# Optimization experiments

Hardware: AMD Instinct MI355X
Metric: run time of the kernel (lower is better)

Reference implementation:

```python
import jax, jax.numpy as jnp
import numpy as np

S, C = 4096, 12            # words per sentence, chars per word
V, NC = 50000, 26          # word vocab, char vocab
E, EC = 1024, 256          # word / char embedding dims
H, HC = 1024, 256          # word / char LSTM hidden dims
T = 64                     # tagset size


def _lstm_step(W_ih, W_hh, b_ih, b_hh, carry, x):
    # PyTorch LSTM gate order: i, f, g, o
    h, c = carry
    gates = x @ W_ih.T + h @ W_hh.T + b_ih + b_hh
    i, f, g, o = jnp.split(gates, 4, axis=-1)
    c = jax.nn.sigmoid(f) * c + jax.nn.sigmoid(i) * jnp.tanh(g)
    h = jax.nn.sigmoid(o) * jnp.tanh(c)
    return (h, c), h


def setup_inputs() -> dict:
    key = jax.random.key(0)
    ks = jax.random.split(key, 16)
    s = 0.02
    return {
        "char_idx": jax.random.randint(ks[0], (S, C), 0, NC),
        "word_idx": jax.random.randint(ks[1], (S,), 0, V),
        "W_emb_word": jax.random.normal(ks[2], (V, E), jnp.float32) * s,
        "W_emb_char": jax.random.normal(ks[3], (NC, EC), jnp.float32) * s,
        "W_ih_c": jax.random.normal(ks[4], (4 * HC, EC), jnp.float32) * s,
        "W_hh_c": jax.random.normal(ks[5], (4 * HC, HC), jnp.float32) * s,
        "b_ih_c": jnp.zeros((4 * HC,), jnp.float32),
        "b_hh_c": jnp.zeros((4 * HC,), jnp.float32),
        "W_ih": jax.random.normal(ks[6], (4 * H, E + HC), jnp.float32) * s,
        "W_hh": jax.random.normal(ks[7], (4 * H, H), jnp.float32) * s,
        "b_ih": jnp.zeros((4 * H,), jnp.float32),
        "b_hh": jnp.zeros((4 * H,), jnp.float32),
        "W_tag": jax.random.normal(ks[8], (T, H), jnp.float32) * s,
        "b_tag": jnp.zeros((T,), jnp.float32),
    }


def reference(char_idx, word_idx, W_emb_word, W_emb_char,
              W_ih_c, W_hh_c, b_ih_c, b_hh_c,
              W_ih, W_hh, b_ih, b_hh, W_tag, b_tag):
    # --- char-level LSTM, batched over all S words at once ---
    char_x = W_emb_char[char_idx]                     # [S, C, EC]
    carry0 = (jnp.zeros((S, HC), char_x.dtype), jnp.zeros((S, HC), char_x.dtype))
    step_c = lambda carry, x: _lstm_step(W_ih_c, W_hh_c, b_ih_c, b_hh_c, carry, x)
    (h_char, _), _ = jax.lax.scan(step_c, carry0, jnp.swapaxes(char_x, 0, 1))  # h_char: [S, HC]

    # --- word-level LSTM over the sentence (batch 1) ---
    word_emb = W_emb_word[word_idx]                   # [S, E]
    x = jnp.concatenate([word_emb, h_char], axis=-1)  # [S, E+HC]
    carry0w = (jnp.zeros((H,), x.dtype), jnp.zeros((H,), x.dtype))
    step_w = lambda carry, xt: _lstm_step(W_ih, W_hh, b_ih, b_hh, carry, xt)
    _, hs = jax.lax.scan(step_w, carry0w, x)          # hs: [S, H]

    tag_space = hs @ W_tag.T + b_tag                  # [S, T]
    return jax.nn.log_softmax(tag_space, axis=1)
```

## Files before the change

kernel.cpp:

```cpp
#include <hip/hip_runtime.h>
#include <hip/hip_bf16.h>

#define SLEN 4096
#define CLEN 12
#define ECD  256
#define HCD  256
#define ED   1024
#define HD   1024
#define TD   64
#define NSLOT 32
#define POLL_LIMIT 2048

typedef unsigned  uv4 __attribute__((ext_vector_type(4)));
typedef __attribute__((ext_vector_type(8))) short bf16x8;
typedef __attribute__((ext_vector_type(4))) float f32x4;

#if defined(__has_builtin)
#if __has_builtin(__builtin_amdgcn_sdot4)
#define HAVE_SDOT4 1
#endif
#if __has_builtin(__builtin_amdgcn_perm)
#define HAVE_PERM 1
#endif
#endif

#ifdef HAVE_PERM
#define PERM2(hi, lo) __builtin_amdgcn_perm((unsigned)(hi), (unsigned)(lo), 0x05040100u)
#else
#define PERM2(hi, lo) ((((unsigned)(lo)) & 0xFFFFu) | (((unsigned)(hi)) << 16))
#endif

#define GLOAD_LDS16(g, l)                                                    \
    __builtin_amdgcn_global_load_lds(                                        \
        (const __attribute__((address_space(1))) void*)(g),                  \
        (__attribute__((address_space(3))) void*)(l), 16, 0, 0)

__device__ __forceinline__ float sigmoidf_(float x) { return 1.f / (1.f + __expf(-x)); }
__device__ __forceinline__ float tanh_fast(float x) {
    float ax = fabsf(x);
    float e = __expf(2.f * ax);
    float t = 1.f - 2.f / (e + 1.f);
    return copysignf(t, x);
}
__device__ __forceinline__ unsigned short bf16r(float f) {
    unsigned u = __float_as_uint(f);
    return (unsigned short)((u + 0x7FFFu + ((u >> 16) & 1u)) >> 16);
}

__global__ __launch_bounds__(256) void prep_all(
    const float* __restrict__ Wih,  unsigned short* __restrict__ Wihb,
    const float* __restrict__ Wec,  const float* __restrict__ Wihc,
    const float* __restrict__ bihc, const float* __restrict__ bhhc,
    float* __restrict__ table,
    const float* __restrict__ Whhc, unsigned short* __restrict__ Wt,
    const float* __restrict__ Wtag, unsigned short* __restrict__ Wtagb,
    unsigned* __restrict__ hdata, int* __restrict__ xcd_ctr,
    const int* __restrict__ word_idx, const float* __restrict__ Wemb,
    unsigned short* __restrict__ Xw)
{
    const int b = blockIdx.x, tid = threadIdx.x;
    if (b < 2560) {
        int i = b * 256 + tid;
        const float4* s = reinterpret_cast<const float4*>(Wih + (size_t)i * 8);
        float4 a = s[0], b2 = s[1];
        unsigned short o[8] = { bf16r(a.x), bf16r(a.y), bf16r(a.z), bf16r(a.w),
                                bf16r(b2.x), bf16r(b2.y), bf16r(b2.z), bf16r(b2.w) };
        *reinterpret_cast<uint4*>(Wihb + (size_t)i * 8) = *reinterpret_cast<uint4*>(o);
    } else if (b < 2664) {
        int id = (b - 2560) * 256 + tid;
        if (id < 26 * 1024) {
            int c = id >> 10, rp = id & 1023;
            int u = rp >> 2, g = rp & 3, row = g * 256 + u;
            const float4* a = reinterpret_cast<const float4*>(Wec + (size_t)c * 256);
            const float4* bb = reinterpret_cast<const float4*>(Wihc + (size_t)row * 256);
            float acc = 0.f;
            #pragma unroll 16
            for (int k = 0; k < 64; ++k) {
                float4 av = a[k], bv = bb[k];
                acc += av.x * bv.x + av.y * bv.y + av.z * bv.z + av.w * bv.w;
            }
            table[id] = acc + bihc[row] + bhhc[row];
        }
    } else if (b < 2792) {
        int id = (b - 2664) * 256 + tid;
        int C = id >> 5, kg = id & 31;
        int h = C >> 9, rem = C & 511, g = rem >> 7, ul = rem & 127;
        int row = g * 256 + h * 128 + ul;
        const float4* sv = reinterpret_cast<const float4*>(
            Whhc + (size_t)row * 256 + kg * 8);
        float4 a = sv[0], b2 = sv[1];
        unsigned short o[8] = { bf16r(a.x), bf16r(a.y), bf16r(a.z), bf16r(a.w),
                                bf16r(b2.x), bf16r(b2.y), bf16r(b2.z), bf16r(b2.w) };
        *reinterpret_cast<uint4*>(Wt + (size_t)(kg * 1024 + C) * 8) =
            *reinterpret_cast<uint4*>(o);
    } else if (b < 2824) {
        int i = (b - 2792) * 256 + tid;
        const float4* s = reinterpret_cast<const float4*>(Wtag + (size_t)i * 8);
        float4 a = s[0], b2 = s[1];
        unsigned short o[8] = { bf16r(a.x), bf16r(a.y), bf16r(a.z), bf16r(a.w),
                                bf16r(b2.x), bf16r(b2.y), bf16r(b2.z), bf16r(b2.w) };
        *reinterpret_cast<uint4*>(Wtagb + (size_t)i * 8) = *reinterpret_cast<uint4*>(o);
    } else if (b < 2856) {
        hdata[(b - 2824) * 256 + tid] = 0xFFFF0000u;
    } else if (b < 4904) {
        int id = (b - 2856) * 256 + tid;
        int row = id >> 7, c8 = id & 127;
        int k = c8 * 8;
        const float4* sv = reinterpret_cast<const float4*>(
            Wemb + (size_t)word_idx[row] * 1024 + k);
        float4 a = sv[0], b2 = sv[1];
        unsigned short o[8] = { bf16r(a.x), bf16r(a.y), bf16r(a.z), bf16r(a.w),
                                bf16r(b2.x), bf16r(b2.y), bf16r(b2.z), bf16r(b2.w) };
        *reinterpret_cast<uint4*>(Xw + (size_t)row * 1280 + k) =
            *reinterpret_cast<uint4*>(o);
    } else {
        if (tid < 8) xcd_ctr[tid] = 0;
    }
}

__global__ __launch_bounds__(256) void char_fused(
    const int* __restrict__ char_idx,
    const unsigned short* __restrict__ Wt,
    const float* __restrict__ table,
    unsigned short* __restrict__ Xw)
{
    __shared__ unsigned short hA[2][8192];
    __shared__ int cidx_s[32 * CLEN];

    const int tid  = threadIdx.x;
    const int lane = tid & 63;
    const int wv   = tid >> 6;
    const int fr   = lane & 15;
    const int fkq  = lane >> 4;
    const int w0   = blockIdx.x * 32;

    for (int e = tid; e < 32 * CLEN; e += 256)
        cidx_s[e] = char_idx[(w0 + (e / CLEN)) * CLEN + (e % CLEN)];
    {
        uint4 z; z.x = z.y = z.z = z.w = 0u;
        for (int e = tid; e < 1024; e += 256)
            *reinterpret_cast<uint4*>(&hA[0][e * 8]) = z;
    }
    __syncthreads();

    float cst[32];
    #pragma unroll
    for (int i = 0; i < 32; ++i) cst[i] = 0.f;

    for (int t = 0; t < CLEN; ++t) {
        const int cur = t & 1, nxt = cur ^ 1;
        #pragma unroll
        for (int h = 0; h < 2; ++h) {
            f32x4 acc[2][8];
            #pragma unroll
            for (int m = 0; m < 2; ++m)
                #pragma unroll
                for (int i = 0; i < 8; ++i) acc[m][i] = f32x4{0.f, 0.f, 0.f, 0.f};

            #pragma unroll
            for (int k0i = 0; k0i < 8; ++k0i) {
                const int kg = k0i * 4 + fkq;
                bf16x8 af[2];
                #pragma unroll
                for (int m = 0; m < 2; ++m) {
                    const int row = m * 16 + fr;
                    af[m] = *reinterpret_cast<const bf16x8*>(
                        &hA[cur][row * 256 + ((kg ^ ((row & 7) << 2)) << 3)]);
                }
                #pragma unroll
                for (int i = 0; i < 8; ++i) {
                    const int T = wv + (i << 2);
                    const int col = h * 512 + T * 16 + fr;
                    const bf16x8 bf = *reinterpret_cast<const bf16x8*>(
                        Wt + (size_t)(kg * 1024 + col) * 8);
                    acc[0][i] = __builtin_amdgcn_mfma_f32_16x16x32_bf16(
                        af[0], bf, acc[0][i], 0, 0, 0);
                    acc[1][i] = __builtin_amdgcn_mfma_f32_16x16x32_bf16(
                        af[1], bf, acc[1][i], 0, 0, 0);
                }
            }

            #pragma unroll
            for (int m = 0; m < 2; ++m) {
                #pragma unroll
                for (int r = 0; r < 4; ++r) {
                    const int wl = m * 16 + (lane >> 4) * 4 + r;
                    const int ci = cidx_s[wl * CLEN + t];
                    #pragma unroll
                    for (int ab = 0; ab < 2; ++ab) {
                        const int u = h * 128 + (wv + 4 * ab) * 16 + fr;
                        const float4 tv = *reinterpret_cast<const float4*>(
                            table + (size_t)ci * 1024 + u * 4);
                        const int cix = ((h * 2 + m) * 2 + ab) * 4 + r;
                        const float gi_ = acc[m][0 + ab][r] + tv.x;
                        const float gf_ = acc[m][2 + ab][r] + tv.y;
                        const float gg_ = acc[m][4 + ab][r] + tv.z;
                        const float go_ = acc[m][6 + ab][r] + tv.w;
                        const float i_ = sigmoidf_(gi_), f_ = sigmoidf_(gf_);
                        const float g_ = tanh_fast(gg_), o_ = sigmoidf_(go_);
                        const float cn = f_ * cst[cix] + i_ * g_;
                        cst[cix] = cn;
                        const unsigned short hb = bf16r(o_ * tanh_fast(cn));
                        const int chn = u >> 3;
                        hA[nxt][wl * 256 + ((chn ^ ((wl & 7) << 2)) << 3) + (u & 7)] = hb;
                    }
                }
            }
        }
        __syncthreads();
    }

    for (int e = tid; e < 1024; e += 256) {
        const int w = e >> 5, ch = e & 31;
        uint4 v = *reinterpret_cast<uint4*>(
            &hA[0][w * 256 + ((ch ^ ((w & 7) << 2)) << 3)]);
        *reinterpret_cast<uint4*>(
            Xw + (size_t)(w0 + w) * 1280 + 1024 + ch * 8) = v;
    }
}

__global__ __launch_bounds__(256) void gemm_bf16_bt(
    const unsigned short* __restrict__ A, const unsigned short* __restrict__ B,
    const float* __restrict__ bias0, const float* __restrict__ bias1,
    float* __restrict__ C, int M, int N, int K)
{
    __shared__ unsigned short As[128 * 64];
    __shared__ unsigned short Bs[128 * 64];
    const int tid  = threadIdx.x;
    const int lane = tid & 63;
    const int wv   = tid >> 6;
    const int wm = wv >> 1, wn = wv & 1;
    const int fr = lane & 15, fk = lane >> 4;
    const int n0 = blockIdx.x * 128;
    const int m0 = blockIdx.y * 128;

    int srcA[4], srcB[4];
    int ldsb[4];
    #pragma unroll
    for (int c = 0; c < 4; ++c) {
        int ch = c * 256 + wv * 64 + lane;
        int row = ch >> 3, chunk = ch & 7;
        int swc = chunk ^ (row & 7);
        srcA[c] = (m0 + row) * K + swc * 8;
        srcB[c] = (n0 + row) * K + swc * 8;
        ldsb[c] = (c * 256 + wv * 64) * 8;
    }

    f32x4 acc[4][4];
    #pragma unroll
    for (int i = 0; i < 4; ++i)
        #pragma unroll
        for (int j = 0; j < 4; ++j) acc[i][j] = f32x4{0.f, 0.f, 0.f, 0.f};

    for (int k0 = 0; k0 < K; k0 += 64) {
        if (k0 > 0) __syncthreads();
        #pragma unroll
        for (int c = 0; c < 4; ++c) {
            GLOAD_LDS16(A + srcA[c] + k0, As + ldsb[c]);
            GLOAD_LDS16(B + srcB[c] + k0, Bs + ldsb[c]);
        }
        asm volatile("s_waitcnt vmcnt(0)" ::: "memory");
        __syncthreads();
        #pragma unroll
        for (int ks = 0; ks < 2; ++ks) {
            bf16x8 af[4], bfr[4];
            #pragma unroll
            for (int i = 0; i < 4; ++i) {
                int ra = wm * 64 + i * 16 + fr;
                af[i] = *reinterpret_cast<const bf16x8*>(
                    &As[ra * 64 + (((ks * 4 + fk) ^ (ra & 7)) << 3)]);
                int rb = wn * 64 + i * 16 + fr;
                bfr[i] = *reinterpret_cast<const bf16x8*>(
                    &Bs[rb * 64 + (((ks * 4 + fk) ^ (rb & 7)) << 3)]);
            }
            #pragma unroll
            for (int i = 0; i < 4; ++i)
                #pragma unroll
                for (int j = 0; j < 4; ++j)
                    acc[i][j] = __builtin_amdgcn_mfma_f32_16x16x32_bf16(
                        af[i], bfr[j], acc[i][j], 0, 0, 0);
        }
    }

    const int colb = n0 + wn * 64 + fr;
    float bsum[4];
    #pragma unroll
    for (int j = 0; j < 4; ++j) bsum[j] = bias0[colb + j * 16] + bias1[colb + j * 16];
    #pragma unroll
    for (int i = 0; i < 4; ++i) {
        int row0 = m0 + wm * 64 + i * 16 + fk * 4;
        #pragma unroll
        for (int j = 0; j < 4; ++j) {
            int col = colb + j * 16;
            #pragma unroll
            for (int r = 0; r < 4; ++r)
                C[(size_t)(row0 + r) * N + col] = acc[i][j][r] + bsum[j];
        }
    }
}

__global__ __launch_bounds__(256, 1) void word_rec(
    const float* __restrict__ precomp, const float* __restrict__ W_hh,
    unsigned* __restrict__ hs_b, unsigned* hdata, int* xcd_ctr)
{
    const int tid  = threadIdx.x;
    const int v    = tid >> 6;
    const int lane = tid & 63;
    const int q    = lane >> 5;
    const int m    = lane & 31;
    const int j    = lane & 7;

    __shared__ int s_vals[2];
    if (tid == 0) {
        unsigned xcc;
        asm volatile("s_getreg_b32 %0, hwreg(HW_REG_XCC_ID)" : "=s"(xcc));
        xcc &= 7u;
        s_vals[0] = (int)xcc;
        s_vals[1] = atomicAdd(&xcd_ctr[xcc], 1);
    }
    __syncthreads();
    const int xcc  = s_vals[0];
    const int slot = s_vals[1];
    if (slot >= NSLOT) return;

    const int base_u = slot * 32 + v * 8;
    unsigned* hdata_x = hdata + xcc * 1024;

    int   wq[16][8];
    float scl[16];
    #pragma unroll
    for (int r = 0; r < 16; ++r) {
        const int grow = (2 * q + (r >> 3)) * 1024 + base_u + (r & 7);
        const float4* rp = reinterpret_cast<const float4*>(
            W_hh + (size_t)grow * 1024 + 32 * m);
        float wv_[32];
        float mx = 0.f;
        #pragma unroll
        for (int d = 0; d < 8; ++d) {
            float4 f = rp[d];
            wv_[4*d+0] = f.x; wv_[4*d+1] = f.y; wv_[4*d+2] = f.z; wv_[4*d+3] = f.w;
            mx = fmaxf(mx, fmaxf(fmaxf(fabsf(f.x), fabsf(f.y)),
                                 fmaxf(fabsf(f.z), fabsf(f.w))));
        }
        mx = fmaxf(mx, __shfl_xor(mx, 1));
        mx = fmaxf(mx, __shfl_xor(mx, 2));
        mx = fmaxf(mx, __shfl_xor(mx, 4));
        mx = fmaxf(mx, __shfl_xor(mx, 8));
        mx = fmaxf(mx, __shfl_xor(mx, 16));
        const float inv = (mx > 0.f) ? (127.f / mx) : 0.f;
        scl[r] = mx * (1.f / (127.f * 127.f));
        #pragma unroll
        for (int d = 0; d < 8; ++d) {
            int b0 = (int)rintf(wv_[4*d+0] * inv) & 255;
            int b1 = (int)rintf(wv_[4*d+1] * inv) & 255;
            int b2 = (int)rintf(wv_[4*d+2] * inv) & 255;
            int b3 = (int)rintf(wv_[4*d+3] * inv) & 255;
            wq[r][d] = b0 | (b1 << 8) | (b2 << 16) | (b3 << 24);
        }
    }

#ifdef HAVE_SDOT4
    #define DOT4(a, b, c) __builtin_amdgcn_sdot4((a), (b), (c), false)
#else
    #define DOT4(a, b, c) ({ int _d; \
        asm("v_dot4_i32_i8 %0, %1, %2, %3" : "=v"(_d) : "v"(a), "v"(b), "v"(c)); _d; })
#endif

    float c_reg = 0.f;

    for (int t = 0; t < SLEN; ++t) {
        const int pp = (t + 1) & 1;
        const int pc = t & 1;

        float pre0 = 0.f, pre1 = 0.f, pre2 = 0.f, pre3 = 0.f;
        if (lane < 8) {
            const float* pr = precomp + (size_t)t * 4096 + base_u + j;
            pre0 = pr[0]; pre1 = pr[1024]; pre2 = pr[2048]; pre3 = pr[3072];
        }

        int hq[8];
        if (t > 0) {
            const unsigned tw = ((unsigned)(t - 1)) << 16;
            const unsigned* dp = hdata_x + pp * 512 + 16 * m;
            uv4 w0_, w1_, w2_, w3_;
            int it = 0; bool dead = false;
            for (;;) {
                asm volatile(
                    "global_load_dwordx4 %0, %4, off sc0\n\t"
                    "global_load_dwordx4 %1, %4, off offset:16 sc0\n\t"
                    "global_load_dwordx4 %2, %4, off offset:32 sc0\n\t"
                    "global_load_dwordx4 %3, %4, off offset:48 sc0\n\t"
                    "s_waitcnt vmcnt(0)"
                    : "=&v"(w0_), "=&v"(w1_), "=&v"(w2_), "=&v"(w3_)
                    : "v"(dp) : "memory");
                unsigned bad =
                    (w0_.x ^ tw) | (w0_.y ^ tw) | (w0_.z ^ tw) | (w0_.w ^ tw) |
                    (w1_.x ^ tw) | (w1_.y ^ tw) | (w1_.z ^ tw) | (w1_.w ^ tw) |
                    (w2_.x ^ tw) | (w2_.y ^ tw) | (w2_.z ^ tw) | (w2_.w ^ tw) |
                    (w3_.x ^ tw) | (w3_.y ^ tw) | (w3_.z ^ tw) | (w3_.w ^ tw);
                if (__all((bad & 0xFFFF0000u) == 0u)) break;
                if (++it > POLL_LIMIT) { dead = true; break; }
            }
            if (dead) return;
            hq[0] = (int)PERM2(w0_.y, w0_.x);
            hq[1] = (int)PERM2(w0_.w, w0_.z);
            hq[2] = (int)PERM2(w1_.y, w1_.x);
            hq[3] = (int)PERM2(w1_.w, w1_.z);
            hq[4] = (int)PERM2(w2_.y, w2_.x);
            hq[5] = (int)PERM2(w2_.w, w2_.z);
            hq[6] = (int)PERM2(w3_.y, w3_.x);
            hq[7] = (int)PERM2(w3_.w, w3_.z);
        } else {
            #pragma unroll
            for (int i = 0; i < 8; ++i) hq[i] = 0;
        }

        float self = 0.f;
        #pragma unroll
        for (int r = 0; r < 16; ++r) {
            int a0 = 0, a1 = 0;
            #pragma unroll
            for (int d = 0; d < 4; ++d) {
                a0 = DOT4(wq[r][d],     hq[d],     a0);
                a1 = DOT4(wq[r][4 + d], hq[4 + d], a1);
            }
            int s = a0 + a1;
            s += __shfl_xor(s, 1);  s += __shfl_xor(s, 2);
            s += __shfl_xor(s, 4);  s += __shfl_xor(s, 8);
            s += __shfl_xor(s, 16);
            self = ((lane & 31) == r) ? (float)s * scl[r] : self;
        }

        const float gi = __shfl(self, j);
        const float gf = __shfl(self, 8 + j);
        const float gg = __shfl(self, 32 + j);
        const float go = __shfl(self, 40 + j);

        float h = 0.f;
        if (lane < 8) {
            const float i_ = sigmoidf_(gi + pre0);
            const float f_ = sigmoidf_(gf + pre1);
            const float g_ = tanh_fast(gg + pre2);
            const float o_ = sigmoidf_(go + pre3);
            c_reg = f_ * c_reg + i_ * g_;
            h = o_ * tanh_fast(c_reg);
        }

        const float hn = __shfl_down(h, 1);
        int qv = (int)rintf(fminf(fmaxf(h * 127.f, -127.f), 127.f));
        const int qn = __shfl(qv, lane | 1);
        if (lane < 8 && (lane & 1) == 0) {
            unsigned pb = (unsigned)bf16r(h) | ((unsigned)bf16r(hn) << 16);
            hs_b[(size_t)t * 512 + (base_u >> 1) + (lane >> 1)] = pb;
            unsigned pk = ((unsigned)t << 16) | ((unsigned)(qn & 255) << 8)
                        | (unsigned)(qv & 255);
            unsigned* dpw = hdata_x + pc * 512 + slot * 16 + v * 4 + (lane >> 1);
            asm volatile("global_store_dword %0, %1, off sc0"
                         :: "v"(dpw), "v"(pk) : "memory");
        }
    }
    #undef DOT4
}

__global__ __launch_bounds__(256) void tag_mfma(
    const unsigned short* __restrict__ A,
    const unsigned short* __restrict__ B,
    const float* __restrict__ btag, float* __restrict__ out)
{
    __shared__ unsigned short As[128 * 64];
    __shared__ unsigned short Bs[64 * 64];
    __shared__ float ts[128 * 65];

    const int tid  = threadIdx.x;
    const int lane = tid & 63;
    const int wm = (tid >> 6) >> 1, wn = (tid >> 6) & 1;
    const int fr = lane & 15, fk = lane >> 4;
    const int m0 = blockIdx.x * 128;

    uint4 ar[4], br[2];
    int rowa[4], kca[4], rowb[2], kcb[2];
    #pragma unroll
    for (int c = 0; c < 4; ++c) {
        int ch = c * 256 + tid;
        rowa[c] = ch >> 3; kca[c] = ch & 7;
    }
    #pragma unroll
    for (int c = 0; c < 2; ++c) {
        int ch = c * 256 + tid;
        rowb[c] = ch >> 3; kcb[c] = ch & 7;
    }

    auto load_tiles = [&](int k0) {
        #pragma unroll
        for (int c = 0; c < 4; ++c)
            ar[c] = *reinterpret_cast<const uint4*>(
                A + (size_t)(m0 + rowa[c]) * 1024 + k0 + kca[c] * 8);
        #pragma unroll
        for (int c = 0; c < 2; ++c)
            br[c] = *reinterpret_cast<const uint4*>(
                B + (size_t)rowb[c] * 1024 + k0 + kcb[c] * 8);
    };

    f32x4 acc[4][2];
    #pragma unroll
    for (int i = 0; i < 4; ++i)
        #pragma unroll
        for (int j = 0; j < 2; ++j) acc[i][j] = f32x4{0.f, 0.f, 0.f, 0.f};

    load_tiles(0);
    for (int k0 = 0; k0 < 1024; k0 += 64) {
        __syncthreads();
        #pragma unroll
        for (int c = 0; c < 4; ++c) {
            int sw = kca[c] ^ (rowa[c] & 7);
            *reinterpret_cast<uint4*>(&As[rowa[c] * 64 + sw * 8]) = ar[c];
        }
        #pragma unroll
        for (int c = 0; c < 2; ++c) {
            int sw = kcb[c] ^ (rowb[c] & 7);
            *reinterpret_cast<uint4*>(&Bs[rowb[c] * 64 + sw * 8]) = br[c];
        }
        __syncthreads();
        if (k0 + 64 < 1024) load_tiles(k0 + 64);
        #pragma unroll
        for (int ks = 0; ks < 2; ++ks) {
            bf16x8 af[4], bfr[2];
            #pragma unroll
            for (int i = 0; i < 4; ++i) {
                int ra = wm * 64 + i * 16 + fr;
                af[i] = *reinterpret_cast<const bf16x8*>(
                    &As[ra * 64 + (((ks * 4 + fk) ^ (ra & 7)) << 3)]);
            }
            #pragma unroll
            for (int j = 0; j < 2; ++j) {
                int rb = wn * 32 + j * 16 + fr;
                bfr[j] = *reinterpret_cast<const bf16x8*>(
                    &Bs[rb * 64 + (((ks * 4 + fk) ^ (rb & 7)) << 3)]);
            }
            #pragma unroll
            for (int i = 0; i < 4; ++i)
                #pragma unroll
                for (int j = 0; j < 2; ++j)
                    acc[i][j] = __builtin_amdgcn_mfma_f32_16x16x32_bf16(
                        af[i], bfr[j], acc[i][j], 0, 0, 0);
        }
    }

    #pragma unroll
    for (int i = 0; i < 4; ++i) {
        int row0 = wm * 64 + i * 16 + fk * 4;
        #pragma unroll
        for (int j = 0; j < 2; ++j) {
            int col = wn * 32 + j * 16 + fr;
            float bt = btag[col];
            #pragma unroll
            for (int r = 0; r < 4; ++r)
                ts[(row0 + r) * 65 + col] = acc[i][j][r] + bt;
        }
    }
    __syncthreads();

    if (tid < 128) {
        const float* rowp = ts + tid * 65;
        float mx = rowp[0];
        #pragma unroll 16
        for (int c = 1; c < 64; ++c) mx = fmaxf(mx, rowp[c]);
        float ssum = 0.f;
        #pragma unroll 16
        for (int c = 0; c < 64; ++c) ssum += __expf(rowp[c] - mx);
        const float lse = mx + logf(ssum);
        float* op = out + (size_t)(m0 + tid) * 64;
        #pragma unroll 16
        for (int c = 0; c < 64; ++c) op[c] = rowp[c] - lse;
    }
}

extern "C" void kernel_launch(void* const* d_in, const int* in_sizes, int n_in,
                              void* d_out, int out_size, void* d_ws, size_t ws_size,
                              hipStream_t stream)
{
    const int*   char_idx = (const int*)  d_in[0];
    const int*   word_idx = (const int*)  d_in[1];
    const float* Wemb     = (const float*)d_in[2];
    const float* Wec      = (const float*)d_in[3];
    const float* Wihc     = (const float*)d_in[4];
    const float* Whhc     = (const float*)d_in[5];
    const float* bihc     = (const float*)d_in[6];
    const float* bhhc     = (const float*)d_in[7];
    const float* Wih      = (const float*)d_in[8];
    const float* Whh      = (const float*)d_in[9];
    const float* bih      = (const float*)d_in[10];
    const float* bhh      = (const float*)d_in[11];
    const float* Wtag     = (const float*)d_in[12];
    const float* btag     = (const float*)d_in[13];
    float* out = (float*)d_out;

    char* w = (char*)d_ws;
    float*          precomp = (float*)w;            w += (size_t)SLEN * 4096 * 4;
    unsigned short* Wihb    = (unsigned short*)w;   w += (size_t)4096 * 1280 * 2;
    unsigned short* Xw      = (unsigned short*)w;   w += (size_t)4096 * 1280 * 2;
    unsigned*       hs_b    = (unsigned*)w;         w += (size_t)SLEN * 512 * 4;
    unsigned short* Wt      = (unsigned short*)w;   w += (size_t)32 * 1024 * 8 * 2;
    float*          table   = (float*)w;            w += 26 * 1024 * 4 + 1920;
    unsigned short* Wtagb   = (unsigned short*)w;   w += (size_t)64 * 1024 * 2;
    unsigned*       hdata   = (unsigned*)w;         w += 8 * 1024 * 4;
    int*            xcd_ctr = (int*)w;

    prep_all<<<4905, 256, 0, stream>>>(Wih, Wihb, Wec, Wihc, bihc, bhhc, table,
                                       Whhc, Wt, Wtag, Wtagb, hdata, xcd_ctr,
                                       word_idx, Wemb, Xw);

    char_fused<<<128, 256, 0, stream>>>(char_idx, Wt, table, Xw);

    gemm_bf16_bt<<<dim3(32, 32), 256, 0, stream>>>(
        Xw, Wihb, bih, bhh, precomp, SLEN, 4096, 1280);

    word_rec<<<256, 256, 0, stream>>>(precomp, Whh, hs_b, hdata, xcd_ctr);

    tag_mfma<<<32, 256, 0, stream>>>(
        (const unsigned short*)hs_b, Wtagb, btag, out);
}
```

Measured before the change: 842.5 us.

## Double-buffer LDS tiles in bf16 GEMM and swizzle block order

Turns the input-projection GEMM's LDS staging into a two-buffer pipeline, so the next K-tile's global-to-LDS loads are issued before computing on the current one. It waits with a partial vmcnt instead of draining all loads. It also remaps block IDs so that groups of blocks share A/B tiles in L2. This doubles LDS use, which may reduce occupancy. The remap hard-codes a 32-column grid and assumes the total block count is divisible by 8.

```diff
diff --git a/kernel.cpp b/kernel.cpp
--- a/kernel.cpp
+++ b/kernel.cpp
@@ -224,15 +224,18 @@
     const float* __restrict__ bias0, const float* __restrict__ bias1,
     float* __restrict__ C, int M, int N, int K)
 {
-    __shared__ unsigned short As[128 * 64];
-    __shared__ unsigned short Bs[128 * 64];
+    __shared__ unsigned short As[2][128 * 64];
+    __shared__ unsigned short Bs[2][128 * 64];
     const int tid  = threadIdx.x;
     const int lane = tid & 63;
     const int wv   = tid >> 6;
     const int wm = wv >> 1, wn = wv & 1;
     const int fr = lane & 15, fk = lane >> 4;
-    const int n0 = blockIdx.x * 128;
-    const int m0 = blockIdx.y * 128;
+
+    const int bid = blockIdx.y * 32 + blockIdx.x;
+    const int bsw = (bid & 7) * 128 + (bid >> 3);
+    const int n0 = (bsw & 31) * 128;
+    const int m0 = (bsw >> 5) * 128;
 
     int srcA[4], srcB[4];
     int ldsb[4];
@@ -246,21 +249,31 @@
         ldsb[c] = (c * 256 + wv * 64) * 8;
     }
 
+    auto stage = [&](int buf, int k0) {
+        #pragma unroll
+        for (int c = 0; c < 4; ++c) {
+            GLOAD_LDS16(A + srcA[c] + k0, &As[buf][ldsb[c]]);
+            GLOAD_LDS16(B + srcB[c] + k0, &Bs[buf][ldsb[c]]);
+        }
+    };
+
     f32x4 acc[4][4];
     #pragma unroll
     for (int i = 0; i < 4; ++i)
         #pragma unroll
         for (int j = 0; j < 4; ++j) acc[i][j] = f32x4{0.f, 0.f, 0.f, 0.f};
 
-    for (int k0 = 0; k0 < K; k0 += 64) {
-        if (k0 > 0) __syncthreads();
-        #pragma unroll
-        for (int c = 0; c < 4; ++c) {
-            GLOAD_LDS16(A + srcA[c] + k0, As + ldsb[c]);
-            GLOAD_LDS16(B + srcB[c] + k0, Bs + ldsb[c]);
-        }
-        asm volatile("s_waitcnt vmcnt(0)" ::: "memory");
-        __syncthreads();
+    const int NT = K / 64;
+    stage(0, 0);
+    for (int kt = 0; kt < NT; ++kt) {
+        const int cur = kt & 1;
+        if (kt + 1 < NT) {
+            stage(cur ^ 1, (kt + 1) * 64);
+            asm volatile("s_waitcnt vmcnt(8)" ::: "memory");
+        } else {
+            asm volatile("s_waitcnt vmcnt(0)" ::: "memory");
+        }
+        __builtin_amdgcn_s_barrier();
         #pragma unroll
         for (int ks = 0; ks < 2; ++ks) {
             bf16x8 af[4], bfr[4];
@@ -268,10 +281,10 @@
             for (int i = 0; i < 4; ++i) {
                 int ra = wm * 64 + i * 16 + fr;
                 af[i] = *reinterpret_cast<const bf16x8*>(
-                    &As[ra * 64 + (((ks * 4 + fk) ^ (ra & 7)) << 3)]);
+                    &As[cur][ra * 64 + (((ks * 4 + fk) ^ (ra & 7)) << 3)]);
                 int rb = wn * 64 + i * 16 + fr;
                 bfr[i] = *reinterpret_cast<const bf16x8*>(
-                    &Bs[rb * 64 + (((ks * 4 + fk) ^ (rb & 7)) << 3)]);
+                    &Bs[cur][rb * 64 + (((ks * 4 + fk) ^ (rb & 7)) << 3)]);
             }
             #pragma unroll
             for (int i = 0; i < 4; ++i)
@@ -280,6 +293,8 @@
                     acc[i][j] = __builtin_amdgcn_mfma_f32_16x16x32_bf16(
                         af[i], bfr[j], acc[i][j], 0, 0, 0);
         }
+        if (kt + 2 < NT)
+            __builtin_amdgcn_s_barrier();
     }
 
     const int colb = n0 + wn * 64 + fr;
```

Result: no change. 831.8 us (-1.3%).
